# Kernel optimization log

Hardware: AMD Instinct MI355X
Metric: run time of the kernel (lower is better)

Reference implementation:

```python
import jax, jax.numpy as jnp
import numpy as np

N = 4096; TD = 768; ID = 512; H = 256; NH = 4; HD = H // NH; NC = 3; E = 131072


def _gcn(x, w, b, src, dst, n):
    # GCNConv: add self loops, sym-normalize, aggregate at dst
    loop = jnp.arange(n)
    s = jnp.concatenate([src, loop])
    d = jnp.concatenate([dst, loop])
    deg = jax.ops.segment_sum(jnp.ones(s.shape[0], x.dtype), d, num_segments=n)
    dinv = jnp.where(deg > 0, jax.lax.rsqrt(deg), 0.0)
    norm = dinv[s] * dinv[d]                      # [E+N]
    h = x @ w                                     # [N,H] transform
    out = jax.ops.segment_sum(norm[:, None] * h[s], d, num_segments=n)
    return out + b


def setup_inputs() -> dict:
    key = jax.random.key(0)
    ks = jax.random.split(key, 20)
    p = lambda k, shp, sc: jax.random.normal(k, shp, jnp.float32) * sc
    inp = {
        "text_features": jax.random.normal(ks[0], (N, TD), jnp.float32),
        "image_features": jax.random.normal(ks[1], (N, ID), jnp.float32),
        "edge_index": jax.random.randint(ks[2], (2, E), 0, N, jnp.int32),
        "text_w": p(ks[3], (TD, H), 0.02), "text_b": jnp.zeros((H,), jnp.float32),
        "image_w": p(ks[4], (ID, H), 0.02), "image_b": jnp.zeros((H,), jnp.float32),
        "wq": p(ks[5], (H, H), 0.02), "bq": jnp.zeros((H,), jnp.float32),
        "wk": p(ks[6], (H, H), 0.02), "bk": jnp.zeros((H,), jnp.float32),
        "wv": p(ks[7], (H, H), 0.02), "bv": jnp.zeros((H,), jnp.float32),
        "wo": p(ks[8], (H, H), 0.02), "bo": jnp.zeros((H,), jnp.float32),
        "gcn1_w": p(ks[9], (H, H), 0.02), "gcn1_b": jnp.zeros((H,), jnp.float32),
        "gcn2_w": p(ks[10], (H, H), 0.02), "gcn2_b": jnp.zeros((H,), jnp.float32),
        "cls_w": p(ks[11], (H, NC), 0.02), "cls_b": jnp.zeros((NC,), jnp.float32),
    }
    return inp


def reference(text_features, image_features, edge_index,
              text_w, text_b, image_w, image_b,
              wq, bq, wk, bk, wv, bv, wo, bo,
              gcn1_w, gcn1_b, gcn2_w, gcn2_b, cls_w, cls_b):
    # fused linear+relu projections, then elementwise fuse of sum
    combined = (jax.nn.relu(text_features @ text_w + text_b)
                + jax.nn.relu(image_features @ image_w + image_b))  # [N,H]
    # MHA over all nodes (seq_len=N, batch=1)
    q = (combined @ wq + bq).reshape(N, NH, HD)
    k = (combined @ wk + bk).reshape(N, NH, HD)
    v = (combined @ wv + bv).reshape(N, NH, HD)
    scores = jnp.einsum('nhd,mhd->hnm', q, k) / jnp.sqrt(jnp.float32(HD))
    attn = jax.nn.softmax(scores, axis=-1)
    o = jnp.einsum('hnm,mhd->nhd', attn, v).reshape(N, H)
    attn_out = o @ wo + bo
    # two GCN layers
    src, dst = edge_index[0], edge_index[1]
    g1 = jax.nn.relu(_gcn(attn_out, gcn1_w, gcn1_b, src, dst, N))
    g2 = _gcn(g1, gcn2_w, gcn2_b, src, dst, N)
    return g2 @ cls_w + cls_b
```

## Files before the change

kernel.cpp:

```cpp
#include <hip/hip_runtime.h>
#include <hip/hip_bf16.h>

typedef unsigned short ushort;
typedef __attribute__((ext_vector_type(8))) short short8;
typedef __attribute__((ext_vector_type(4))) short short4v;
typedef __attribute__((ext_vector_type(4))) float f32x4;

constexpr int N_  = 4096;
constexpr int TD_ = 768;
constexpr int ID_ = 512;
constexpr int H_  = 256;
constexpr int HD_ = 64;
constexpr int E_  = 131072;
constexpr int SPLITS = 8;
constexpr float QSCALE = 0.125f * 1.44269504088896f;

#define MFMA16(a, b, c) __builtin_amdgcn_mfma_f32_16x16x32_bf16(a, b, c, 0, 0, 0)

__device__ inline ushort f2bf(float x) {
    union { float f; unsigned u; } v; v.f = x;
    unsigned r = v.u + 0x7fff + ((v.u >> 16) & 1);
    return (ushort)(r >> 16);
}
__device__ inline float lo2f(unsigned u) { union { unsigned x; float f; } v; v.x = u << 16; return v.f; }
__device__ inline float hi2f(unsigned u) { union { unsigned x; float f; } v; v.x = u & 0xffff0000u; return v.f; }

__device__ inline float exp2r(float x) {
    float r;
    asm("v_exp_f32 %0, %1" : "=v"(r) : "v"(x));
    return r;
}
__device__ inline unsigned pkbf(float lo, float hi) {
    union { float f; unsigned u; } a, b; a.f = lo; b.f = hi;
    return __builtin_amdgcn_perm(b.u + 0x8000u, a.u + 0x8000u, 0x07060302u);
}

__device__ inline void gl_lds16(const void* g, void* l) {
    __builtin_amdgcn_global_load_lds((const __attribute__((address_space(1))) unsigned int*)g,
                                     (__attribute__((address_space(3))) unsigned int*)l, 16, 0, 0);
}

__device__ inline void stage64(const ushort* g, long long strideEl, ushort* lds, int w, int l) {
    int r8 = l >> 3;
    int cc = (l & 7) ^ r8;
    #pragma unroll
    for (int p = 0; p < 2; p++) {
        int row = w * 16 + p * 8 + r8;
        gl_lds16(g + (long long)row * strideEl + cc * 8, lds + (w * 16 + p * 8) * 64);
    }
}
__device__ inline int swz(int row, int kOff) {
    return row * 64 + ((((kOff >> 3) ^ (row & 7))) << 3);
}


__global__ __launch_bounds__(256) void k_init(int* __restrict__ indeg, int* __restrict__ pos) {
    int i = blockIdx.x * 256 + threadIdx.x;
    indeg[i] = 0;
    pos[i] = 0;
}

__global__ __launch_bounds__(256) void k_count(const int* __restrict__ dst, int* __restrict__ indeg) {
    int e = blockIdx.x * 256 + threadIdx.x;
    atomicAdd(&indeg[dst[e]], 1);
}

__global__ __launch_bounds__(1024) void k_scan(const int* __restrict__ indeg, int* __restrict__ offs,
                                               float* __restrict__ dinv) {
    __shared__ int sums[1024];
    int t = threadIdx.x;
    int b = t * 4;
    int a0 = indeg[b], a1 = indeg[b + 1], a2 = indeg[b + 2], a3 = indeg[b + 3];
    int s = a0 + a1 + a2 + a3;
    sums[t] = s;
    __syncthreads();
    for (int off = 1; off < 1024; off <<= 1) {
        int vv = (t >= off) ? sums[t - off] : 0;
        __syncthreads();
        sums[t] += vv;
        __syncthreads();
    }
    int excl = sums[t] - s;
    offs[b]     = excl;
    offs[b + 1] = excl + a0;
    offs[b + 2] = excl + a0 + a1;
    offs[b + 3] = excl + a0 + a1 + a2;
    dinv[b]     = 1.f / sqrtf((float)(a0 + 1));
    dinv[b + 1] = 1.f / sqrtf((float)(a1 + 1));
    dinv[b + 2] = 1.f / sqrtf((float)(a2 + 1));
    dinv[b + 3] = 1.f / sqrtf((float)(a3 + 1));
}

__global__ __launch_bounds__(256) void k_scatter(const int* __restrict__ src, const int* __restrict__ dst,
                                                 const int* __restrict__ offs, const float* __restrict__ dinv,
                                                 int* __restrict__ pos, int* __restrict__ ssrc,
                                                 float* __restrict__ sw) {
    int e = blockIdx.x * 256 + threadIdx.x;
    int s = src[e], d = dst[e];
    int p = atomicAdd(&pos[d], 1);
    int idx = offs[d] + p;
    ssrc[idx] = s;
    sw[idx] = dinv[s] * dinv[d];
}


__global__ __launch_bounds__(256) void k_prep(const float* __restrict__ text, const float* __restrict__ img,
                                              const float* __restrict__ tw, const float* __restrict__ iw,
                                              const float* __restrict__ wq, const float* __restrict__ wk,
                                              const float* __restrict__ wv, const float* __restrict__ wo,
                                              const float* __restrict__ g1w, const float* __restrict__ g2w,
                                              ushort* __restrict__ textbf, ushort* __restrict__ imgbf,
                                              ushort* __restrict__ wobf,
                                              ushort* __restrict__ twT, ushort* __restrict__ iwT,
                                              ushort* __restrict__ wqT, ushort* __restrict__ wkT,
                                              ushort* __restrict__ wvT, ushort* __restrict__ g1wT,
                                              ushort* __restrict__ g2wT) {
    __shared__ float Ts[64][65];
    const int b = blockIdx.x;
    const int t = threadIdx.x;
    if (b < 2592) {
        size_t base = ((size_t)b * 256 + t) * 8;
        const size_t TXE = (size_t)N_ * TD_, IME = (size_t)N_ * ID_;
        const float* src; ushort* dst;
        if (base < TXE) { src = text + base; dst = textbf + base; }
        else if (base < TXE + IME) { src = img + (base - TXE); dst = imgbf + (base - TXE); }
        else { src = wo + (base - TXE - IME); dst = wobf + (base - TXE - IME); }
        float4 x = *(const float4*)src;
        float4 y = *(const float4*)(src + 4);
        ushort o[8] = { f2bf(x.x), f2bf(x.y), f2bf(x.z), f2bf(x.w),
                        f2bf(y.x), f2bf(y.y), f2bf(y.z), f2bf(y.w) };
        *(short8*)dst = *(const short8*)o;
        return;
    }
    int wb = b - 2592;
    const float* src; ushort* dst; int R, tile;
    if (wb < 48)       { src = tw;  dst = twT;  R = 768; tile = wb; }
    else if (wb < 80)  { src = iw;  dst = iwT;  R = 512; tile = wb - 48; }
    else if (wb < 96)  { src = wq;  dst = wqT;  R = 256; tile = wb - 80; }
    else if (wb < 112) { src = wk;  dst = wkT;  R = 256; tile = wb - 96; }
    else if (wb < 128) { src = wv;  dst = wvT;  R = 256; tile = wb - 112; }
    else if (wb < 144) { src = g1w; dst = g1wT; R = 256; tile = wb - 128; }
    else               { src = g2w; dst = g2wT; R = 256; tile = wb - 144; }
    const int r0 = (tile >> 2) * 64, c0 = (tile & 3) * 64;
    #pragma unroll
    for (int u = 0; u < 16; u++) {
        int lin = t + u * 256;
        int r = lin >> 6, c = lin & 63;
        Ts[r][c] = src[(size_t)(r0 + r) * 256 + c0 + c];
    }
    __syncthreads();
    #pragma unroll
    for (int u = 0; u < 16; u++) {
        int lin = t + u * 256;
        int c = lin >> 6, r = lin & 63;
        dst[(size_t)(c0 + c) * R + r0 + r] = f2bf(Ts[r][c]);
    }
}


__global__ __launch_bounds__(256) void k_foldw(const ushort* __restrict__ g1wT, const ushort* __restrict__ wobf,
                                               const float* __restrict__ bo,
                                               ushort* __restrict__ WpT, float* __restrict__ bp) {
    __shared__ ushort As[2][4096];
    __shared__ ushort Bs[2][4096];
    __shared__ ushort Cs[64 * 72];
    const int t = threadIdx.x;
    if (blockIdx.x == 16) {
        float acc = 0.f;
        const ushort* row = g1wT + (size_t)t * 256;
        for (int m8 = 0; m8 < 256; m8 += 8) {
            #pragma unroll
            for (int j = 0; j < 8; j++) acc += bo[m8 + j] * lo2f(((unsigned)row[m8 + j]) << 16);
        }
        bp[t] = acc;
        return;
    }
    const int bm = (blockIdx.x >> 2) * 64, bn = (blockIdx.x & 3) * 64;
    const int w = t >> 6, l = t & 63, q = l >> 4, i = l & 15;
    f32x4 acc[4];
    #pragma unroll
    for (int nt = 0; nt < 4; nt++) acc[nt] = (f32x4){0, 0, 0, 0};
    stage64(g1wT + (size_t)bm * H_, H_, As[0], w, l);
    stage64(wobf + (size_t)bn * H_, H_, Bs[0], w, l);
    for (int c = 0; c < 4; c++) {
        __syncthreads();
        if (c < 3) {
            stage64(g1wT + (size_t)bm * H_ + (c + 1) * 64, H_, As[(c + 1) & 1], w, l);
            stage64(wobf + (size_t)bn * H_ + (c + 1) * 64, H_, Bs[(c + 1) & 1], w, l);
        }
        const ushort* Ab = As[c & 1];
        const ushort* Bb = Bs[c & 1];
        #pragma unroll
        for (int kb = 0; kb < 2; kb++) {
            short8 af = *(const short8*)&Ab[swz(w * 16 + i, kb * 32 + q * 8)];
            #pragma unroll
            for (int nt = 0; nt < 4; nt++) {
                short8 bfr = *(const short8*)&Bb[swz(nt * 16 + i, kb * 32 + q * 8)];
                acc[nt] = MFMA16(af, bfr, acc[nt]);
            }
        }
    }
    __syncthreads();
    #pragma unroll
    for (int nt = 0; nt < 4; nt++)
        #pragma unroll
        for (int r = 0; r < 4; r++)
            Cs[(w * 16 + q * 4 + r) * 72 + nt * 16 + i] = f2bf(acc[nt][r]);
    __syncthreads();
    int rr = t >> 2, c16 = (t & 3) * 16;
    short8 v0 = *(const short8*)&Cs[rr * 72 + c16];
    short8 v1 = *(const short8*)&Cs[rr * 72 + c16 + 8];
    ushort* dst = WpT + (size_t)(bm + rr) * H_ + bn + c16;
    *(short8*)dst = v0;
    *(short8*)(dst + 8) = v1;
}


__global__ __launch_bounds__(256) void k_combined_mfma(const ushort* __restrict__ text, const ushort* __restrict__ img,
                                                       const ushort* __restrict__ twT, const ushort* __restrict__ iwT,
                                                       const float* __restrict__ tb, const float* __restrict__ ib,
                                                       ushort* __restrict__ out) {
    __shared__ ushort As[2][64 * 64];
    __shared__ ushort Bs[2][64 * 64];
    __shared__ ushort Cs[64 * 72];
    const int bm = blockIdx.x * 64, bn = blockIdx.y * 64;
    const int t = threadIdx.x, w = t >> 6, l = t & 63, q = l >> 4, i = l & 15;
    constexpr int NCH = 20;

    auto stageC = [&](int c, int buf) {
        if (c < 12) {
            stage64(text + (size_t)bm * TD_ + c * 64, TD_, As[buf], w, l);
            stage64(twT + (size_t)bn * TD_ + c * 64, TD_, Bs[buf], w, l);
        } else {
            int cc = c - 12;
            stage64(img + (size_t)bm * ID_ + cc * 64, ID_, As[buf], w, l);
            stage64(iwT + (size_t)bn * ID_ + cc * 64, ID_, Bs[buf], w, l);
        }
    };

    f32x4 acc1[4], acc2[4];
    #pragma unroll
    for (int nt = 0; nt < 4; nt++) { acc1[nt] = (f32x4){0,0,0,0}; acc2[nt] = (f32x4){0,0,0,0}; }

    stageC(0, 0);
    for (int c = 0; c < NCH; c++) {
        __syncthreads();
        if (c + 1 < NCH) stageC(c + 1, (c + 1) & 1);
        const ushort* Ab = As[c & 1];
        const ushort* Bb = Bs[c & 1];
        f32x4* acc = (c < 12) ? acc1 : acc2;
        #pragma unroll
        for (int kb = 0; kb < 2; kb++) {
            short8 af = *(const short8*)&Ab[swz(w * 16 + i, kb * 32 + q * 8)];
            #pragma unroll
            for (int nt = 0; nt < 4; nt++) {
                short8 bfr = *(const short8*)&Bb[swz(nt * 16 + i, kb * 32 + q * 8)];
                acc[nt] = MFMA16(af, bfr, acc[nt]);
            }
        }
    }
    __syncthreads();
    #pragma unroll
    for (int nt = 0; nt < 4; nt++) {
        float b1 = tb[bn + nt * 16 + i], b2 = ib[bn + nt * 16 + i];
        #pragma unroll
        for (int r = 0; r < 4; r++) {
            float v = fmaxf(acc1[nt][r] + b1, 0.f) + fmaxf(acc2[nt][r] + b2, 0.f);
            Cs[(w * 16 + q * 4 + r) * 72 + nt * 16 + i] = f2bf(v);
        }
    }
    __syncthreads();
    int rr = t >> 2, c16 = (t & 3) * 16;
    short8 v0 = *(const short8*)&Cs[rr * 72 + c16];
    short8 v1 = *(const short8*)&Cs[rr * 72 + c16 + 8];
    ushort* dst = out + (size_t)(bm + rr) * H_ + bn + c16;
    *(short8*)dst = v0;
    *(short8*)(dst + 8) = v1;
}


__global__ __launch_bounds__(256) void k_qkv_mfma(const ushort* __restrict__ A,
                                                  const ushort* __restrict__ WqT, const ushort* __restrict__ WkT,
                                                  const ushort* __restrict__ WvT,
                                                  const float* __restrict__ bq, const float* __restrict__ bk,
                                                  const float* __restrict__ bv,
                                                  ushort* __restrict__ Qg, ushort* __restrict__ Kg,
                                                  ushort* __restrict__ Vtg) {
    __shared__ ushort As[2][64 * 64];
    __shared__ ushort Bs[2][64 * 64];
    __shared__ ushort Cs[64 * 72];
    const int bm = blockIdx.x * 64, head = blockIdx.y, z = blockIdx.z;
    const ushort* WT = (z == 0) ? WqT : (z == 1) ? WkT : WvT;
    const float* bias = (z == 0) ? bq : (z == 1) ? bk : bv;
    const int t = threadIdx.x, w = t >> 6, l = t & 63, q = l >> 4, i = l & 15;
    f32x4 acc[4];
    #pragma unroll
    for (int nt = 0; nt < 4; nt++) acc[nt] = (f32x4){0,0,0,0};

    stage64(A + (size_t)bm * H_, H_, As[0], w, l);
    stage64(WT + (size_t)(head * 64) * H_, H_, Bs[0], w, l);
    for (int c = 0; c < 4; c++) {
        __syncthreads();
        if (c < 3) {
            stage64(A + (size_t)bm * H_ + (c + 1) * 64, H_, As[(c + 1) & 1], w, l);
            stage64(WT + (size_t)(head * 64) * H_ + (c + 1) * 64, H_, Bs[(c + 1) & 1], w, l);
        }
        const ushort* Ab = As[c & 1];
        const ushort* Bb = Bs[c & 1];
        #pragma unroll
        for (int kb = 0; kb < 2; kb++) {
            short8 af = *(const short8*)&Ab[swz(w * 16 + i, kb * 32 + q * 8)];
            #pragma unroll
            for (int nt = 0; nt < 4; nt++) {
                short8 bfr = *(const short8*)&Bb[swz(nt * 16 + i, kb * 32 + q * 8)];
                acc[nt] = MFMA16(af, bfr, acc[nt]);
            }
        }
    }
    __syncthreads();
    #pragma unroll
    for (int nt = 0; nt < 4; nt++) {
        float bv_ = bias[head * 64 + nt * 16 + i];
        #pragma unroll
        for (int r = 0; r < 4; r++) {
            float v = acc[nt][r] + bv_;
            if (z == 0) v *= QSCALE;
            if (z < 2) Cs[(w * 16 + q * 4 + r) * 72 + nt * 16 + i] = f2bf(v);
            else       Cs[(nt * 16 + i) * 72 + w * 16 + q * 4 + r] = f2bf(v);
        }
    }
    __syncthreads();
    int rr = t >> 2, c16 = (t & 3) * 16;
    short8 v0 = *(const short8*)&Cs[rr * 72 + c16];
    short8 v1 = *(const short8*)&Cs[rr * 72 + c16 + 8];
    ushort* dst;
    if (z < 2) dst = ((z == 0) ? Qg : Kg) + (size_t)head * N_ * HD_ + (size_t)(bm + rr) * HD_ + c16;
    else       dst = Vtg + (size_t)head * HD_ * N_ + (size_t)rr * N_ + bm + c16;
    *(short8*)dst = v0;
    *(short8*)(dst + 8) = v1;
}


__global__ __launch_bounds__(256) void k_attn_mfma(const ushort* __restrict__ Qg, const ushort* __restrict__ Kg,
                                                   const ushort* __restrict__ Vtg, ushort* __restrict__ Op,
                                                   float* __restrict__ lp) {
    __shared__ ushort Ks[4096];
    __shared__ ushort Vs[4096];
    __shared__ ushort Ps[4][16 * 72];
    const int head = blockIdx.y, r0 = blockIdx.x * 64, z = blockIdx.z;
    const int t = threadIdx.x, w = t >> 6, l = t & 63, q = l >> 4, i = l & 15;
    const int rw = (i ^ (i >> 1)) & 7;
    ushort* Pw = &Ps[w][0];

    short8 qf[2];
    #pragma unroll
    for (int kb = 0; kb < 2; kb++)
        qf[kb] = *(const short8*)(Qg + ((size_t)head * N_ + r0 + w * 16 + i) * HD_ + kb * 32 + q * 8);

    f32x4 Oacc[4];
    float lacc = 0.f;
    #pragma unroll
    for (int dt = 0; dt < 4; dt++) Oacc[dt] = (f32x4){0, 0, 0, 0};

    const int NT = 64 / SPLITS;
    const int cb0 = z * NT;
    for (int it = 0; it < NT; it++) {
        const int cb = cb0 + it;
        __syncthreads();
        stage64(Kg + ((size_t)head * N_ + (size_t)cb * 64) * HD_, HD_, Ks, w, l);
        stage64(Vtg + (size_t)head * HD_ * N_ + cb * 64, N_, Vs, w, l);
        __syncthreads();

        f32x4 St[4];
        #pragma unroll
        for (int kt = 0; kt < 4; kt++) St[kt] = (f32x4){0, 0, 0, 0};
        #pragma unroll
        for (int kb = 0; kb < 2; kb++) {
            #pragma unroll
            for (int kt = 0; kt < 4; kt++) {
                short8 kf = *(const short8*)&Ks[swz(kt * 16 + i, kb * 32 + q * 8)];
                St[kt] = MFMA16(kf, qf[kb], St[kt]);
            }
        }

        #pragma unroll
        for (int kt = 0; kt < 4; kt++) {
            float p0 = exp2r(St[kt][0]), p1 = exp2r(St[kt][1]);
            float p2 = exp2r(St[kt][2]), p3 = exp2r(St[kt][3]);
            lacc += (p0 + p1) + (p2 + p3);
            int off = i * 72 + (((2 * kt + (q >> 1)) ^ rw) << 3) + ((q & 1) << 2);
            uint2 v; v.x = pkbf(p0, p1); v.y = pkbf(p2, p3);
            *(uint2*)&Pw[off] = v;
        }

        #pragma unroll
        for (int kb = 0; kb < 2; kb++) {
            short8 pf = *(const short8*)&Pw[i * 72 + (((4 * kb + q) ^ rw) << 3)];
            #pragma unroll
            for (int dt = 0; dt < 4; dt++) {
                short8 vf = *(const short8*)&Vs[swz(dt * 16 + i, kb * 32 + q * 8)];
                Oacc[dt] = MFMA16(vf, pf, Oacc[dt]);
            }
        }
    }

    lacc += __shfl_xor(lacc, 16);
    lacc += __shfl_xor(lacc, 32);

    const size_t sh = ((size_t)z * 4 + head) * N_;
    const int row = r0 + w * 16 + i;
    #pragma unroll
    for (int dt = 0; dt < 4; dt++) {
        uint2 v;
        v.x = pkbf(Oacc[dt][0], Oacc[dt][1]);
        v.y = pkbf(Oacc[dt][2], Oacc[dt][3]);
        *(uint2*)&Op[(sh + row) * HD_ + dt * 16 + q * 4] = v;
    }
    if (l < 16) lp[sh + r0 + w * 16 + l] = lacc;
}

__global__ __launch_bounds__(256) void k_attn_merge(const ushort* __restrict__ Op, const float* __restrict__ lp,
                                                    ushort* __restrict__ obuf) {
    const int t = threadIdx.x;
    const int idx = blockIdx.x * 16 + (t >> 4);
    const int h = idx >> 12, n = idx & 4095;
    const int d4 = (t & 15) * 4;
    float lsum = 0.f;
    float acc[4] = {0.f, 0.f, 0.f, 0.f};
    #pragma unroll
    for (int s = 0; s < SPLITS; s++) {
        size_t sh = ((size_t)s * 4 + h) * N_ + n;
        lsum += lp[sh];
        uint2 o4 = *(const uint2*)&Op[sh * HD_ + d4];
        acc[0] += lo2f(o4.x); acc[1] += hi2f(o4.x);
        acc[2] += lo2f(o4.y); acc[3] += hi2f(o4.y);
    }
    float inv = 1.f / lsum;
    uint2 res;
    res.x = pkbf(acc[0] * inv, acc[1] * inv);
    res.y = pkbf(acc[2] * inv, acc[3] * inv);
    *(uint2*)&obuf[(size_t)n * H_ + h * HD_ + d4] = res;
}


template <bool BIAS>
__global__ __launch_bounds__(256) void k_gemm_bf16(const ushort* __restrict__ A, const ushort* __restrict__ BT,
                                                   const float* __restrict__ bias, ushort* __restrict__ outb) {
    __shared__ ushort As[2][4096];
    __shared__ ushort Bs[2][4096];
    __shared__ ushort Cs[64 * 72];
    const int bm = blockIdx.x * 64, bn = blockIdx.y * 64;
    const int t = threadIdx.x, w = t >> 6, l = t & 63, q = l >> 4, i = l & 15;
    f32x4 acc[4];
    #pragma unroll
    for (int nt = 0; nt < 4; nt++) acc[nt] = (f32x4){0, 0, 0, 0};

    stage64(A + (size_t)bm * H_, H_, As[0], w, l);
    stage64(BT + (size_t)bn * H_, H_, Bs[0], w, l);
    for (int c = 0; c < 4; c++) {
        __syncthreads();
        if (c < 3) {
            stage64(A + (size_t)bm * H_ + (c + 1) * 64, H_, As[(c + 1) & 1], w, l);
            stage64(BT + (size_t)bn * H_ + (c + 1) * 64, H_, Bs[(c + 1) & 1], w, l);
        }
        const ushort* Ab = As[c & 1];
        const ushort* Bb = Bs[c & 1];
        #pragma unroll
        for (int kb = 0; kb < 2; kb++) {
            short8 af = *(const short8*)&Ab[swz(w * 16 + i, kb * 32 + q * 8)];
            #pragma unroll
            for (int nt = 0; nt < 4; nt++) {
                short8 bfr = *(const short8*)&Bb[swz(nt * 16 + i, kb * 32 + q * 8)];
                acc[nt] = MFMA16(af, bfr, acc[nt]);
            }
        }
    }
    __syncthreads();
    #pragma unroll
    for (int nt = 0; nt < 4; nt++) {
        float bb = BIAS ? bias[bn + nt * 16 + i] : 0.f;
        #pragma unroll
        for (int r = 0; r < 4; r++)
            Cs[(w * 16 + q * 4 + r) * 72 + nt * 16 + i] = f2bf(acc[nt][r] + bb);
    }
    __syncthreads();
    int rr = t >> 2, c16 = (t & 3) * 16;
    short8 v0 = *(const short8*)&Cs[rr * 72 + c16];
    short8 v1 = *(const short8*)&Cs[rr * 72 + c16 + 8];
    ushort* dst = outb + (size_t)(bm + rr) * H_ + bn + c16;
    *(short8*)dst = v0;
    *(short8*)(dst + 8) = v1;
}


__global__ __launch_bounds__(256) void k_agg1(const ushort* __restrict__ h, const int* __restrict__ ssrc,
                                              const float* __restrict__ sw, const int* __restrict__ offs,
                                              const int* __restrict__ indeg, const float* __restrict__ dinv,
                                              const float* __restrict__ bias, ushort* __restrict__ outb) {
    const int t = threadIdx.x;
    const int j = blockIdx.x * 4 + (t >> 6);
    const int d0 = (t & 63) * 4;
    float dj = dinv[j];
    uint2 hv = *(const uint2*)&h[(size_t)j * H_ + d0];
    float s2 = dj * dj;
    float a0 = s2 * lo2f(hv.x), a1 = s2 * hi2f(hv.x), a2 = s2 * lo2f(hv.y), a3 = s2 * hi2f(hv.y);
    int start = offs[j], cnt = indeg[j];
    for (int e = 0; e < cnt; e++) {
        int s = ssrc[start + e];
        float wg = sw[start + e];
        uint2 v = *(const uint2*)&h[(size_t)s * H_ + d0];
        a0 += wg * lo2f(v.x); a1 += wg * hi2f(v.x);
        a2 += wg * lo2f(v.y); a3 += wg * hi2f(v.y);
    }
    a0 = fmaxf(a0 + bias[d0], 0.f);
    a1 = fmaxf(a1 + bias[d0 + 1], 0.f);
    a2 = fmaxf(a2 + bias[d0 + 2], 0.f);
    a3 = fmaxf(a3 + bias[d0 + 3], 0.f);
    uint2 o;
    o.x = pkbf(a0, a1);
    o.y = pkbf(a2, a3);
    *(uint2*)&outb[(size_t)j * H_ + d0] = o;
}


__global__ __launch_bounds__(256) void k_aggcls(const ushort* __restrict__ h, const int* __restrict__ ssrc,
                                                const float* __restrict__ sw, const int* __restrict__ offs,
                                                const int* __restrict__ indeg, const float* __restrict__ dinv,
                                                const float* __restrict__ bias, const float* __restrict__ cw,
                                                const float* __restrict__ cb, float* __restrict__ out) {
    const int t = threadIdx.x;
    const int j = blockIdx.x * 4 + (t >> 6);
    const int lane = t & 63;
    const int d0 = lane * 4;
    float dj = dinv[j];
    uint2 hv = *(const uint2*)&h[(size_t)j * H_ + d0];
    float s2 = dj * dj;
    float a0 = s2 * lo2f(hv.x), a1 = s2 * hi2f(hv.x), a2 = s2 * lo2f(hv.y), a3 = s2 * hi2f(hv.y);
    int start = offs[j], cnt = indeg[j];
    for (int e = 0; e < cnt; e++) {
        int s = ssrc[start + e];
        float wg = sw[start + e];
        uint2 v = *(const uint2*)&h[(size_t)s * H_ + d0];
        a0 += wg * lo2f(v.x); a1 += wg * hi2f(v.x);
        a2 += wg * lo2f(v.y); a3 += wg * hi2f(v.y);
    }
    a0 += bias[d0]; a1 += bias[d0 + 1]; a2 += bias[d0 + 2]; a3 += bias[d0 + 3];
    float p0 = 0.f, p1 = 0.f, p2 = 0.f;
    #pragma unroll
    for (int r = 0; r < 4; r++) {
        float g = (r == 0) ? a0 : (r == 1) ? a1 : (r == 2) ? a2 : a3;
        p0 += g * cw[(d0 + r) * 3 + 0];
        p1 += g * cw[(d0 + r) * 3 + 1];
        p2 += g * cw[(d0 + r) * 3 + 2];
    }
    #pragma unroll
    for (int off = 32; off > 0; off >>= 1) {
        p0 += __shfl_xor(p0, off);
        p1 += __shfl_xor(p1, off);
        p2 += __shfl_xor(p2, off);
    }
    if (lane == 0) {
        out[j * 3 + 0] = p0 + cb[0];
        out[j * 3 + 1] = p1 + cb[1];
        out[j * 3 + 2] = p2 + cb[2];
    }
}


extern "C" void kernel_launch(void* const* d_in, const int* in_sizes, int n_in,
                              void* d_out, int out_size, void* d_ws, size_t ws_size,
                              hipStream_t stream) {
    const float* text = (const float*)d_in[0];
    const float* img  = (const float*)d_in[1];
    const int*   eidx = (const int*)d_in[2];
    const float* tw  = (const float*)d_in[3];
    const float* tb  = (const float*)d_in[4];
    const float* iw  = (const float*)d_in[5];
    const float* ib  = (const float*)d_in[6];
    const float* wq  = (const float*)d_in[7];
    const float* bq  = (const float*)d_in[8];
    const float* wk  = (const float*)d_in[9];
    const float* bk  = (const float*)d_in[10];
    const float* wv  = (const float*)d_in[11];
    const float* bv  = (const float*)d_in[12];
    const float* wo  = (const float*)d_in[13];
    const float* bo  = (const float*)d_in[14];
    const float* g1w = (const float*)d_in[15];
    const float* g1b = (const float*)d_in[16];
    const float* g2w = (const float*)d_in[17];
    const float* g2b = (const float*)d_in[18];
    const float* cw  = (const float*)d_in[19];
    const float* cbv = (const float*)d_in[20];

    char* W = (char*)d_ws;
    size_t cur = 0;
    auto alloc = [&](size_t sz) { char* p = W + cur; cur += (sz + 255) & ~(size_t)255; return p; };

    float* dinv  = (float*)alloc(N_ * 4);
    float* swv   = (float*)alloc(E_ * 4);
    int* indeg   = (int*)alloc(N_ * 4);
    int* offs    = (int*)alloc(N_ * 4);
    int* pos     = (int*)alloc(N_ * 4);
    int* ssrc    = (int*)alloc(E_ * 4);
    ushort* Qg   = (ushort*)alloc((size_t)N_ * H_ * 2);
    ushort* Kg   = (ushort*)alloc((size_t)N_ * H_ * 2);
    ushort* Vtg  = (ushort*)alloc((size_t)N_ * H_ * 2);
    ushort* obuf = (ushort*)alloc((size_t)N_ * H_ * 2);
    ushort* WpT  = (ushort*)alloc((size_t)H_ * H_ * 2);
    float* bp    = (float*)alloc(H_ * 4);
    ushort* g1wT = (ushort*)alloc((size_t)H_ * H_ * 2);
    ushort* g2wT = (ushort*)alloc((size_t)H_ * H_ * 2);
    ushort* wobf = (ushort*)alloc((size_t)H_ * H_ * 2);
    float* lp    = (float*)alloc((size_t)SPLITS * 4 * N_ * 4);
    char* S = W + cur;

    ushort* textbf = (ushort*)S;
    ushort* imgbf  = textbf + (size_t)N_ * TD_;
    ushort* twT    = imgbf + (size_t)N_ * ID_;
    ushort* iwT    = twT + (size_t)TD_ * H_;
    ushort* wqT    = iwT + (size_t)ID_ * H_;
    ushort* wkT    = wqT + (size_t)H_ * H_;
    ushort* wvT    = wkT + (size_t)H_ * H_;
    ushort* combbf = wvT + (size_t)H_ * H_;
    ushort* Op = (ushort*)S;
    ushort* hbuf  = (ushort*)S;
    ushort* g1b16 = (ushort*)(S + (size_t)2 * 1024 * 1024);
    ushort* hbuf2 = (ushort*)(S + (size_t)4 * 1024 * 1024);

    const int* esrc = eidx;
    const int* edst = eidx + E_;

    k_init<<<dim3(N_ / 256), dim3(256), 0, stream>>>(indeg, pos);
    k_count<<<dim3(E_ / 256), dim3(256), 0, stream>>>(edst, indeg);
    k_scan<<<dim3(1), dim3(1024), 0, stream>>>(indeg, offs, dinv);
    k_scatter<<<dim3(E_ / 256), dim3(256), 0, stream>>>(esrc, edst, offs, dinv, pos, ssrc, swv);

    k_prep<<<dim3(2752), dim3(256), 0, stream>>>(text, img, tw, iw, wq, wk, wv, wo, g1w, g2w,
                                                 textbf, imgbf, wobf, twT, iwT, wqT, wkT, wvT, g1wT, g2wT);
    k_foldw<<<dim3(17), dim3(256), 0, stream>>>(g1wT, wobf, bo, WpT, bp);

    k_combined_mfma<<<dim3(64, 4), dim3(256), 0, stream>>>(textbf, imgbf, twT, iwT, tb, ib, combbf);
    k_qkv_mfma<<<dim3(64, 4, 3), dim3(256), 0, stream>>>(combbf, wqT, wkT, wvT, bq, bk, bv, Qg, Kg, Vtg);
    k_attn_mfma<<<dim3(64, 4, SPLITS), dim3(256), 0, stream>>>(Qg, Kg, Vtg, Op, lp);
    k_attn_merge<<<dim3(1024), dim3(256), 0, stream>>>(Op, lp, obuf);

    k_gemm_bf16<true><<<dim3(64, 4), dim3(256), 0, stream>>>(obuf, WpT, bp, hbuf);
    k_agg1<<<dim3(N_ / 4), dim3(256), 0, stream>>>(hbuf, ssrc, swv, offs, indeg, dinv, g1b, g1b16);
    k_gemm_bf16<false><<<dim3(64, 4), dim3(256), 0, stream>>>(g1b16, g2wT, nullptr, hbuf2);
    k_aggcls<<<dim3(N_ / 4), dim3(256), 0, stream>>>(hbuf2, ssrc, swv, offs, indeg, dinv, g2b, cw, cbv,
                                                     (float*)d_out);
}
```

Measured before the change: 256.1 us.

## Shrink GEMM output tiles to 64x16 for more blocks; fold edge count into prep

The combined-projection GEMM and the two GCN transform GEMMs now compute 64x16 output tiles per block instead of 64x64. This raises the grid from 256 to 1024 blocks so more compute units are busy, and adds a launch-bounds occupancy hint. The cost is re-staging the A tile once for every 16 output columns, four times as often as before. The in-degree atomic count now runs as extra blocks of the prep kernel, which removes one kernel launch. The result is the same either way.

Measured after the change: 239.5 us. 1.07x faster.

```diff
diff --git a/kernel.cpp b/kernel.cpp
--- a/kernel.cpp
+++ b/kernel.cpp
@@ -3,7 +3,6 @@
 
 typedef unsigned short ushort;
 typedef __attribute__((ext_vector_type(8))) short short8;
-typedef __attribute__((ext_vector_type(4))) short short4v;
 typedef __attribute__((ext_vector_type(4))) float f32x4;
 
 constexpr int N_  = 4096;
@@ -49,6 +48,14 @@
         gl_lds16(g + (long long)row * strideEl + cc * 8, lds + (w * 16 + p * 8) * 64);
     }
 }
+__device__ inline void stageB16(const ushort* g, long long strideEl, ushort* lds, int w, int l) {
+    if (w < 2) {
+        int r8 = l >> 3;
+        int row = w * 8 + r8;
+        int cc = (l & 7) ^ (row & 7);
+        gl_lds16(g + (long long)row * strideEl + cc * 8, lds + w * 512);
+    }
+}
 __device__ inline int swz(int row, int kOff) {
     return row * 64 + ((((kOff >> 3) ^ (row & 7))) << 3);
 }
@@ -58,11 +65,6 @@
     int i = blockIdx.x * 256 + threadIdx.x;
     indeg[i] = 0;
     pos[i] = 0;
-}
-
-__global__ __launch_bounds__(256) void k_count(const int* __restrict__ dst, int* __restrict__ indeg) {
-    int e = blockIdx.x * 256 + threadIdx.x;
-    atomicAdd(&indeg[dst[e]], 1);
 }
 
 __global__ __launch_bounds__(1024) void k_scan(const int* __restrict__ indeg, int* __restrict__ offs,
@@ -109,6 +111,7 @@
                                               const float* __restrict__ wq, const float* __restrict__ wk,
                                               const float* __restrict__ wv, const float* __restrict__ wo,
                                               const float* __restrict__ g1w, const float* __restrict__ g2w,
+                                              const int* __restrict__ edst, int* __restrict__ indeg,
                                               ushort* __restrict__ textbf, ushort* __restrict__ imgbf,
                                               ushort* __restrict__ wobf,
                                               ushort* __restrict__ twT, ushort* __restrict__ iwT,
@@ -118,6 +121,11 @@
     __shared__ float Ts[64][65];
     const int b = blockIdx.x;
     const int t = threadIdx.x;
+    if (b >= 2752) {
+        int e = (b - 2752) * 256 + t;
+        atomicAdd(&indeg[edst[e]], 1);
+        return;
+    }
     if (b < 2592) {
         size_t base = ((size_t)b * 256 + t) * 8;
         const size_t TXE = (size_t)N_ * TD_, IME = (size_t)N_ * ID_;
@@ -216,66 +224,51 @@
 }
 
 
-__global__ __launch_bounds__(256) void k_combined_mfma(const ushort* __restrict__ text, const ushort* __restrict__ img,
+__global__ __launch_bounds__(256, 4) void k_combined16(const ushort* __restrict__ text, const ushort* __restrict__ img,
                                                        const ushort* __restrict__ twT, const ushort* __restrict__ iwT,
                                                        const float* __restrict__ tb, const float* __restrict__ ib,
                                                        ushort* __restrict__ out) {
-    __shared__ ushort As[2][64 * 64];
-    __shared__ ushort Bs[2][64 * 64];
-    __shared__ ushort Cs[64 * 72];
-    const int bm = blockIdx.x * 64, bn = blockIdx.y * 64;
+    __shared__ ushort As[2][4096];
+    __shared__ ushort Bs[2][1024];
+    __shared__ ushort Cs[64 * 24];
+    const int bm = blockIdx.x * 64, bn = blockIdx.y * 16;
     const int t = threadIdx.x, w = t >> 6, l = t & 63, q = l >> 4, i = l & 15;
-    constexpr int NCH = 20;
-
-    auto stageC = [&](int c, int buf) {
+    f32x4 acc1 = {0, 0, 0, 0}, acc2 = {0, 0, 0, 0};
+    auto stC = [&](int c, int buf) {
         if (c < 12) {
             stage64(text + (size_t)bm * TD_ + c * 64, TD_, As[buf], w, l);
-            stage64(twT + (size_t)bn * TD_ + c * 64, TD_, Bs[buf], w, l);
+            stageB16(twT + (size_t)bn * TD_ + c * 64, TD_, Bs[buf], w, l);
         } else {
-            int cc = c - 12;
-            stage64(img + (size_t)bm * ID_ + cc * 64, ID_, As[buf], w, l);
-            stage64(iwT + (size_t)bn * ID_ + cc * 64, ID_, Bs[buf], w, l);
+            stage64(img + (size_t)bm * ID_ + (c - 12) * 64, ID_, As[buf], w, l);
+            stageB16(iwT + (size_t)bn * ID_ + (c - 12) * 64, ID_, Bs[buf], w, l);
         }
     };
-
-    f32x4 acc1[4], acc2[4];
-    #pragma unroll
-    for (int nt = 0; nt < 4; nt++) { acc1[nt] = (f32x4){0,0,0,0}; acc2[nt] = (f32x4){0,0,0,0}; }
-
-    stageC(0, 0);
-    for (int c = 0; c < NCH; c++) {
-        __syncthreads();
-        if (c + 1 < NCH) stageC(c + 1, (c + 1) & 1);
+    stC(0, 0);
+    for (int c = 0; c < 20; c++) {
+        __syncthreads();
+        if (c + 1 < 20) stC(c + 1, (c + 1) & 1);
         const ushort* Ab = As[c & 1];
         const ushort* Bb = Bs[c & 1];
-        f32x4* acc = (c < 12) ? acc1 : acc2;
         #pragma unroll
         for (int kb = 0; kb < 2; kb++) {
             short8 af = *(const short8*)&Ab[swz(w * 16 + i, kb * 32 + q * 8)];
-            #pragma unroll
-            for (int nt = 0; nt < 4; nt++) {
-                short8 bfr = *(const short8*)&Bb[swz(nt * 16 + i, kb * 32 + q * 8)];
-                acc[nt] = MFMA16(af, bfr, acc[nt]);
-            }
-        }
-    }
-    __syncthreads();
-    #pragma unroll
-    for (int nt = 0; nt < 4; nt++) {
-        float b1 = tb[bn + nt * 16 + i], b2 = ib[bn + nt * 16 + i];
-        #pragma unroll
-        for (int r = 0; r < 4; r++) {
-            float v = fmaxf(acc1[nt][r] + b1, 0.f) + fmaxf(acc2[nt][r] + b2, 0.f);
-            Cs[(w * 16 + q * 4 + r) * 72 + nt * 16 + i] = f2bf(v);
-        }
-    }
-    __syncthreads();
-    int rr = t >> 2, c16 = (t & 3) * 16;
-    short8 v0 = *(const short8*)&Cs[rr * 72 + c16];
-    short8 v1 = *(const short8*)&Cs[rr * 72 + c16 + 8];
-    ushort* dst = out + (size_t)(bm + rr) * H_ + bn + c16;
-    *(short8*)dst = v0;
-    *(short8*)(dst + 8) = v1;
+            short8 bfr = *(const short8*)&Bb[swz(i, kb * 32 + q * 8)];
+            if (c < 12) acc1 = MFMA16(af, bfr, acc1);
+            else        acc2 = MFMA16(af, bfr, acc2);
+        }
+    }
+    __syncthreads();
+    float b1 = tb[bn + i], b2 = ib[bn + i];
+    #pragma unroll
+    for (int r = 0; r < 4; r++) {
+        float v = fmaxf(acc1[r] + b1, 0.f) + fmaxf(acc2[r] + b2, 0.f);
+        Cs[(w * 16 + q * 4 + r) * 24 + i] = f2bf(v);
+    }
+    __syncthreads();
+    if (t < 128) {
+        int row = t >> 1, h8 = (t & 1) * 8;
+        *(short8*)(out + (size_t)(bm + row) * H_ + bn + h8) = *(const short8*)&Cs[row * 24 + h8];
+    }
 }
 
 
@@ -286,8 +279,8 @@
                                                   const float* __restrict__ bv,
                                                   ushort* __restrict__ Qg, ushort* __restrict__ Kg,
                                                   ushort* __restrict__ Vtg) {
-    __shared__ ushort As[2][64 * 64];
-    __shared__ ushort Bs[2][64 * 64];
+    __shared__ ushort As[2][4096];
+    __shared__ ushort Bs[2][4096];
     __shared__ ushort Cs[64 * 72];
     const int bm = blockIdx.x * 64, head = blockIdx.y, z = blockIdx.z;
     const ushort* WT = (z == 0) ? WqT : (z == 1) ? WkT : WvT;
@@ -382,7 +375,6 @@
                 St[kt] = MFMA16(kf, qf[kb], St[kt]);
             }
         }
-
         #pragma unroll
         for (int kt = 0; kt < 4; kt++) {
             float p0 = exp2r(St[kt][0]), p1 = exp2r(St[kt][1]);
@@ -392,7 +384,6 @@
             uint2 v; v.x = pkbf(p0, p1); v.y = pkbf(p2, p3);
             *(uint2*)&Pw[off] = v;
         }
-
         #pragma unroll
         for (int kb = 0; kb < 2; kb++) {
             short8 pf = *(const short8*)&Pw[i * 72 + (((4 * kb + q) ^ rw) << 3)];
@@ -444,52 +435,41 @@
 
 
 template <bool BIAS>
-__global__ __launch_bounds__(256) void k_gemm_bf16(const ushort* __restrict__ A, const ushort* __restrict__ BT,
+__global__ __launch_bounds__(256, 4) void k_gemm16(const ushort* __restrict__ A, const ushort* __restrict__ BT,
                                                    const float* __restrict__ bias, ushort* __restrict__ outb) {
     __shared__ ushort As[2][4096];
-    __shared__ ushort Bs[2][4096];
-    __shared__ ushort Cs[64 * 72];
-    const int bm = blockIdx.x * 64, bn = blockIdx.y * 64;
+    __shared__ ushort Bs[2][1024];
+    __shared__ ushort Cs[64 * 24];
+    const int bm = blockIdx.x * 64, bn = blockIdx.y * 16;
     const int t = threadIdx.x, w = t >> 6, l = t & 63, q = l >> 4, i = l & 15;
-    f32x4 acc[4];
-    #pragma unroll
-    for (int nt = 0; nt < 4; nt++) acc[nt] = (f32x4){0, 0, 0, 0};
-
+    f32x4 acc = {0, 0, 0, 0};
     stage64(A + (size_t)bm * H_, H_, As[0], w, l);
-    stage64(BT + (size_t)bn * H_, H_, Bs[0], w, l);
+    stageB16(BT + (size_t)bn * H_, H_, Bs[0], w, l);
     for (int c = 0; c < 4; c++) {
         __syncthreads();
         if (c < 3) {
             stage64(A + (size_t)bm * H_ + (c + 1) * 64, H_, As[(c + 1) & 1], w, l);
-            stage64(BT + (size_t)bn * H_ + (c + 1) * 64, H_, Bs[(c + 1) & 1], w, l);
+            stageB16(BT + (size_t)bn * H_ + (c + 1) * 64, H_, Bs[(c + 1) & 1], w, l);
         }
         const ushort* Ab = As[c & 1];
         const ushort* Bb = Bs[c & 1];
         #pragma unroll
         for (int kb = 0; kb < 2; kb++) {
             short8 af = *(const short8*)&Ab[swz(w * 16 + i, kb * 32 + q * 8)];
-            #pragma unroll
-            for (int nt = 0; nt < 4; nt++) {
-                short8 bfr = *(const short8*)&Bb[swz(nt * 16 + i, kb * 32 + q * 8)];
-                acc[nt] = MFMA16(af, bfr, acc[nt]);
-            }
-        }
-    }
-    __syncthreads();
-    #pragma unroll
-    for (int nt = 0; nt < 4; nt++) {
-        float bb = BIAS ? bias[bn + nt * 16 + i] : 0.f;
-        #pragma unroll
-        for (int r = 0; r < 4; r++)
-            Cs[(w * 16 + q * 4 + r) * 72 + nt * 16 + i] = f2bf(acc[nt][r] + bb);
-    }
-    __syncthreads();
-    int rr = t >> 2, c16 = (t & 3) * 16;
-    short8 v0 = *(const short8*)&Cs[rr * 72 + c16];
-    short8 v1 = *(const short8*)&Cs[rr * 72 + c16 + 8];
-    ushort* dst = outb + (size_t)(bm + rr) * H_ + bn + c16;
-    *(short8*)dst = v0;
-    *(short8*)(dst + 8) = v1;
+            short8 bfr = *(const short8*)&Bb[swz(i, kb * 32 + q * 8)];
+            acc = MFMA16(af, bfr, acc);
+        }
+    }
+    __syncthreads();
+    float bb = BIAS ? bias[bn + i] : 0.f;
+    #pragma unroll
+    for (int r = 0; r < 4; r++)
+        Cs[(w * 16 + q * 4 + r) * 24 + i] = f2bf(acc[r] + bb);
+    __syncthreads();
+    if (t < 128) {
+        int row = t >> 1, h8 = (t & 1) * 8;
+        *(short8*)(outb + (size_t)(bm + row) * H_ + bn + h8) = *(const short8*)&Cs[row * 24 + h8];
+    }
 }
 
 
@@ -545,14 +525,12 @@
         a2 += wg * lo2f(v.y); a3 += wg * hi2f(v.y);
     }
     a0 += bias[d0]; a1 += bias[d0 + 1]; a2 += bias[d0 + 2]; a3 += bias[d0 + 3];
-    float p0 = 0.f, p1 = 0.f, p2 = 0.f;
-    #pragma unroll
-    for (int r = 0; r < 4; r++) {
-        float g = (r == 0) ? a0 : (r == 1) ? a1 : (r == 2) ? a2 : a3;
-        p0 += g * cw[(d0 + r) * 3 + 0];
-        p1 += g * cw[(d0 + r) * 3 + 1];
-        p2 += g * cw[(d0 + r) * 3 + 2];
-    }
+    float p0 = a0 * cw[d0 * 3 + 0] + a1 * cw[(d0 + 1) * 3 + 0]
+             + a2 * cw[(d0 + 2) * 3 + 0] + a3 * cw[(d0 + 3) * 3 + 0];
+    float p1 = a0 * cw[d0 * 3 + 1] + a1 * cw[(d0 + 1) * 3 + 1]
+             + a2 * cw[(d0 + 2) * 3 + 1] + a3 * cw[(d0 + 3) * 3 + 1];
+    float p2 = a0 * cw[d0 * 3 + 2] + a1 * cw[(d0 + 1) * 3 + 2]
+             + a2 * cw[(d0 + 2) * 3 + 2] + a3 * cw[(d0 + 3) * 3 + 2];
     #pragma unroll
     for (int off = 32; off > 0; off >>= 1) {
         p0 += __shfl_xor(p0, off);
@@ -631,22 +609,21 @@
     const int* edst = eidx + E_;
 
     k_init<<<dim3(N_ / 256), dim3(256), 0, stream>>>(indeg, pos);
-    k_count<<<dim3(E_ / 256), dim3(256), 0, stream>>>(edst, indeg);
+    k_prep<<<dim3(3264), dim3(256), 0, stream>>>(text, img, tw, iw, wq, wk, wv, wo, g1w, g2w,
+                                                 edst, indeg,
+                                                 textbf, imgbf, wobf, twT, iwT, wqT, wkT, wvT, g1wT, g2wT);
     k_scan<<<dim3(1), dim3(1024), 0, stream>>>(indeg, offs, dinv);
     k_scatter<<<dim3(E_ / 256), dim3(256), 0, stream>>>(esrc, edst, offs, dinv, pos, ssrc, swv);
-
-    k_prep<<<dim3(2752), dim3(256), 0, stream>>>(text, img, tw, iw, wq, wk, wv, wo, g1w, g2w,
-                                                 textbf, imgbf, wobf, twT, iwT, wqT, wkT, wvT, g1wT, g2wT);
     k_foldw<<<dim3(17), dim3(256), 0, stream>>>(g1wT, wobf, bo, WpT, bp);
 
-    k_combined_mfma<<<dim3(64, 4), dim3(256), 0, stream>>>(textbf, imgbf, twT, iwT, tb, ib, combbf);
+    k_combined16<<<dim3(64, 16), dim3(256), 0, stream>>>(textbf, imgbf, twT, iwT, tb, ib, combbf);
     k_qkv_mfma<<<dim3(64, 4, 3), dim3(256), 0, stream>>>(combbf, wqT, wkT, wvT, bq, bk, bv, Qg, Kg, Vtg);
     k_attn_mfma<<<dim3(64, 4, SPLITS), dim3(256), 0, stream>>>(Qg, Kg, Vtg, Op, lp);
     k_attn_merge<<<dim3(1024), dim3(256), 0, stream>>>(Op, lp, obuf);
 
-    k_gemm_bf16<true><<<dim3(64, 4), dim3(256), 0, stream>>>(obuf, WpT, bp, hbuf);
+    k_gemm16<true><<<dim3(64, 16), dim3(256), 0, stream>>>(obuf, WpT, bp, hbuf);
     k_agg1<<<dim3(N_ / 4), dim3(256), 0, stream>>>(hbuf, ssrc, swv, offs, indeg, dinv, g1b, g1b16);
-    k_gemm_bf16<false><<<dim3(64, 4), dim3(256), 0, stream>>>(g1b16, g2wT, nullptr, hbuf2);
+    k_gemm16<false><<<dim3(64, 16), dim3(256), 0, stream>>>(g1b16, g2wT, nullptr, hbuf2);
     k_aggcls<<<dim3(N_ / 4), dim3(256), 0, stream>>>(hbuf2, ssrc, swv, offs, indeg, dinv, g2b, cw, cbv,
                                                      (float*)d_out);
 }
```
